# Kernel optimization log

Hardware: AMD Instinct MI355X
Metric: run time of the kernel (lower is better)

Reference implementation:

```python
import jax, jax.numpy as jnp
import numpy as np

B, Z, H, W, C = 8, 16, 32, 32, 512
C8 = C // 8
N = Z * H * W
EPS = 1e-3  # Keras BatchNormalization default epsilon


def setup_inputs() -> dict:
    key = jax.random.key(0)
    ks = jax.random.split(key, 8)
    scale = 0.05
    x = jax.random.normal(ks[0], (B, Z, H, W, C), jnp.float32)
    return {
        "x": x,
        "bn1_gamma": jnp.ones((C,), jnp.float32),
        "bn1_beta": jnp.zeros((C,), jnp.float32),
        "bn1_mean": jax.random.normal(ks[1], (C,), jnp.float32) * 0.1,
        "bn1_var": jnp.abs(jax.random.normal(ks[2], (C,), jnp.float32)) * 0.1 + 1.0,
        "wq": jax.random.normal(ks[3], (C, C8), jnp.float32) * scale,
        "bq": jnp.zeros((C8,), jnp.float32),
        "wk": jax.random.normal(ks[4], (C, C8), jnp.float32) * scale,
        "bk": jnp.zeros((C8,), jnp.float32),
        "wv": jax.random.normal(ks[5], (C, C8), jnp.float32) * scale,
        "bv": jnp.zeros((C8,), jnp.float32),
        "wp": jax.random.normal(ks[6], (C8, C), jnp.float32) * scale,
        "bp": jnp.zeros((C,), jnp.float32),
        "bn2_gamma": jnp.ones((C,), jnp.float32),
        "bn2_beta": jnp.zeros((C,), jnp.float32),
        "bn2_mean": jax.random.normal(ks[7], (C,), jnp.float32) * 0.1,
        "bn2_var": jnp.ones((C,), jnp.float32),
    }


def _bn(t, gamma, beta, mean, var):
    # Keras BatchNormalization (inference), channels-last axis=-1
    return (t - mean) * jax.lax.rsqrt(var + EPS) * gamma + beta


def _conv1x1(t, w, b):
    # 1x1x1 Conv3D == per-voxel channel matmul
    return jnp.einsum('bzhwc,cd->bzhwd', t, w) + b


def reference(x, bn1_gamma, bn1_beta, bn1_mean, bn1_var,
              wq, bq, wk, bk, wv, bv, wp, bp,
              bn2_gamma, bn2_beta, bn2_mean, bn2_var):
    img = _bn(x, bn1_gamma, bn1_beta, bn1_mean, bn1_var)
    q = _conv1x1(img, wq, bq).reshape(B, N, C8)  # (B, N, c)
    k = _conv1x1(img, wk, bk).reshape(B, N, C8)  # (B, N, c)
    v = _conv1x1(img, wv, bv).reshape(B, N, C8)  # (B, N, c)
    # Keras Dot(axes=[1,2])([q, permute(k)]): contracts the N axis of both
    # -> channel Gram matrix s[b,i,j] = sum_n q[b,n,i] * k[b,n,j]
    s = jnp.einsum('bni,bnj->bij', q, k)          # (B, c, c)
    beta = jax.nn.softmax(s, axis=-1)             # (B, c, c)
    # Keras Dot(axes=[1,2])([beta, v]): attn[b,i,j] = sum_m beta[b,m,i] * v[b,j,m]
    attn = jnp.einsum('bmi,bjm->bij', beta, v)    # (B, c, N)
    # Keras Reshape((Z,H,W,c)) on (B, c, N): row-major reinterpretation
    out = attn.reshape(B, Z, H, W, C8)
    out = _conv1x1(out, wp, bp)                   # (B, Z, H, W, C)
    out = _bn(out, bn2_gamma, bn2_beta, bn2_mean, bn2_var)
    return out
```

## Files before the change

kernel.cpp:

```cpp
#include <hip/hip_runtime.h>

#define EPS 1e-3f

typedef _Float16 f16;
typedef _Float16 f16x8 __attribute__((ext_vector_type(8)));
typedef _Float16 f16x4 __attribute__((ext_vector_type(4)));
typedef float f32x4 __attribute__((ext_vector_type(4)));

constexpr int Bn = 8, C = 512, C8 = 64;
constexpr int N = 16384;
constexpr int M = Bn * N;

constexpr size_t OFF_WHI  = 0;
constexpr size_t OFF_WLO  = 196608;
constexpr size_t OFF_BQKV = 327680;
constexpr size_t OFF_WPT  = 328704;
constexpr size_t OFF_BOUT = 394240;
constexpr size_t OFF_V    = 396288;
constexpr size_t OFF_S    = OFF_V + (size_t)M * 64 * 2;
constexpr size_t OFF_BT   = OFF_S + (size_t)8 * 8 * 4096 * 4;

__global__ __launch_bounds__(256) void k0_fold(
    const float* g1, const float* be1, const float* mu1, const float* va1,
    const float* wq, const float* bq, const float* wk, const float* bk,
    const float* wv, const float* bv, const float* wp, const float* bp,
    const float* g2, const float* be2, const float* mu2, const float* va2,
    char* ws)
{
  f16* whi = (f16*)(ws + OFF_WHI);
  f16* wlo = (f16*)(ws + OFF_WLO);
  float* bqkv = (float*)(ws + OFF_BQKV);
  f16* wpt = (f16*)(ws + OFF_WPT);
  float* bout = (float*)(ws + OFF_BOUT);
  float* sbuf = (float*)(ws + OFF_S);
  __shared__ float red[256];
  int blk = blockIdx.x, t = threadIdx.x;
  if (blk < 192) {
    const float* w; const float* bb; int col;
    if (blk < 64)       { w = wq; bb = bq; col = blk; }
    else if (blk < 128) { w = wk; bb = bk; col = blk - 64; }
    else                { w = wv; bb = bv; col = blk - 128; }
    float part = 0.f;
    for (int c = t; c < 512; c += 256) {
      float a1 = g1[c] * rsqrtf(va1[c] + EPS);
      float d1 = be1[c] - mu1[c] * a1;
      float wval = w[c * 64 + col];
      float fw = a1 * wval;
      f16 hi = (f16)fw;
      whi[blk * 512 + c] = hi;
      if (blk < 128) wlo[blk * 512 + c] = (f16)((fw - (float)hi) * 2048.0f);
      part += d1 * wval;
    }
    red[t] = part; __syncthreads();
    for (int s = 128; s > 0; s >>= 1) { if (t < s) red[t] += red[t + s]; __syncthreads(); }
    if (t == 0) bqkv[blk] = red[0] + bb[col];
  } else {
    int co = blk - 192;
    float a2 = g2[co] * rsqrtf(va2[co] + EPS);
    if (t < 64) wpt[co * 64 + t] = (f16)(wp[t * 512 + co] * a2);
    if (t == 0) bout[co] = (bp[co] - mu2[co]) * a2 + be2[co];
    sbuf[co * 512 + t] = 0.0f;
    sbuf[co * 512 + 256 + t] = 0.0f;
  }
}

__global__ __launch_bounds__(256, 2) void k1_qkv(const float* __restrict__ x, char* __restrict__ ws)
{
  const f16* whi = (const f16*)(ws + OFF_WHI);
  const f16* wlo = (const f16*)(ws + OFF_WLO);
  const float* bqkv = (const float*)(ws + OFF_BQKV);
  f16* vbuf  = (f16*)(ws + OFF_V);
  float* spart = (float*)(ws + OFF_S);

  __shared__ f16 xs[2][64 * 72];

  int t = threadIdx.x;
  int wave = t >> 6, lane = t & 63;
  int m0 = blockIdx.x * 64;

  int srow = t >> 2, scol = (t & 3) * 4;
  const float* xg = x + (size_t)(m0 + srow) * 512 + scol;

  int bn0 = wave * 16 + (lane & 15);
  int bn1 = bn0 + 64;
  int bn2 = bn0 + 128;
  int klane = (lane >> 4) * 8;

  f32x4 acc_h[4][2], acc_l[4][2], acc_v[4];
  for (int i = 0; i < 4; i++) {
    for (int j = 0; j < 2; j++) { acc_h[i][j] = (f32x4){0.f,0.f,0.f,0.f}; acc_l[i][j] = (f32x4){0.f,0.f,0.f,0.f}; }
    acc_v[i] = (f32x4){0.f,0.f,0.f,0.f};
  }

  f32x4 a0 = *(const f32x4*)(xg);
  f32x4 a1 = *(const f32x4*)(xg + 16);
  f32x4 a2 = *(const f32x4*)(xg + 32);
  f32x4 a3 = *(const f32x4*)(xg + 48);

  for (int iter = 0; iter < 8; iter++) {
    f16* xb = &xs[iter & 1][0];
    {
      f16x4 h0, h1, h2, h3;
      for (int e = 0; e < 4; e++) { h0[e]=(f16)a0[e]; h1[e]=(f16)a1[e]; h2[e]=(f16)a2[e]; h3[e]=(f16)a3[e]; }
      *(f16x4*)&xb[srow * 72 + scol     ] = h0;
      *(f16x4*)&xb[srow * 72 + scol + 16] = h1;
      *(f16x4*)&xb[srow * 72 + scol + 32] = h2;
      *(f16x4*)&xb[srow * 72 + scol + 48] = h3;
    }
    __syncthreads();
    if (iter < 7) {
      const float* xi = xg + (iter + 1) * 64;
      a0 = *(const f32x4*)(xi);
      a1 = *(const f32x4*)(xi + 16);
      a2 = *(const f32x4*)(xi + 32);
      a3 = *(const f32x4*)(xi + 48);
    }
    for (int ks = 0; ks < 2; ks++) {
      int kg = iter * 64 + ks * 32 + klane;
      f16x8 b0h = *(const f16x8*)(whi + bn0 * 512 + kg);
      f16x8 b1h = *(const f16x8*)(whi + bn1 * 512 + kg);
      f16x8 b2h = *(const f16x8*)(whi + bn2 * 512 + kg);
      f16x8 b0l = *(const f16x8*)(wlo + bn0 * 512 + kg);
      f16x8 b1l = *(const f16x8*)(wlo + bn1 * 512 + kg);
      int aoff = (lane & 15) * 72 + ks * 32 + klane;
      for (int mt = 0; mt < 4; mt++) {
        f16x8 af = *(const f16x8*)&xb[mt * 16 * 72 + aoff];
        acc_h[mt][0] = __builtin_amdgcn_mfma_f32_16x16x32_f16(af, b0h, acc_h[mt][0], 0, 0, 0);
        acc_h[mt][1] = __builtin_amdgcn_mfma_f32_16x16x32_f16(af, b1h, acc_h[mt][1], 0, 0, 0);
        acc_l[mt][0] = __builtin_amdgcn_mfma_f32_16x16x32_f16(af, b0l, acc_l[mt][0], 0, 0, 0);
        acc_l[mt][1] = __builtin_amdgcn_mfma_f32_16x16x32_f16(af, b1l, acc_l[mt][1], 0, 0, 0);
        acc_v[mt]    = __builtin_amdgcn_mfma_f32_16x16x32_f16(af, b2h, acc_v[mt],    0, 0, 0);
      }
    }
  }

  const float inv2048 = 1.0f / 2048.0f;
  float bA = bqkv[bn0], bB = bqkv[bn1], bV = bqkv[bn2];
  f16* qT = &xs[0][0];
  f16* kT = &xs[1][0];
  __syncthreads();
  for (int mt = 0; mt < 4; mt++)
    for (int r = 0; r < 4; r++) {
      int n = (lane >> 4) * 4 + mt * 16 + r;
      size_t row = (size_t)(m0 + n);
      float qv = acc_h[mt][0][r] + acc_l[mt][0][r] * inv2048 + bA;
      float kv = acc_h[mt][1][r] + acc_l[mt][1][r] * inv2048 + bB;
      qT[bn0 * 72 + n] = (f16)qv;
      kT[bn0 * 72 + n] = (f16)kv;
      vbuf[row * 64 + bn0] = (f16)(acc_v[mt][r] + bV);
    }
  __syncthreads();

  f32x4 gacc[4];
  for (int i = 0; i < 4; i++) gacc[i] = (f32x4){0.f,0.f,0.f,0.f};
  for (int ks = 0; ks < 2; ks++) {
    f16x8 bfr = *(const f16x8*)&kT[(wave * 16 + (lane & 15)) * 72 + ks * 32 + klane];
    for (int it = 0; it < 4; it++) {
      f16x8 afr = *(const f16x8*)&qT[(it * 16 + (lane & 15)) * 72 + ks * 32 + klane];
      gacc[it] = __builtin_amdgcn_mfma_f32_16x16x32_f16(afr, bfr, gacc[it], 0, 0, 0);
    }
  }
  int b = blockIdx.x >> 8;
  int g = blockIdx.x & 7;
  float* sdst = spart + ((size_t)(g * 8 + b)) * 4096;
  int j = wave * 16 + (lane & 15);
  for (int it = 0; it < 4; it++)
    for (int r = 0; r < 4; r++) {
      int i = it * 16 + (lane >> 4) * 4 + r;
      atomicAdd(&sdst[i * 64 + j], gacc[it][r]);
    }
}

__global__ __launch_bounds__(256) void k2b_softmax(char* __restrict__ ws)
{
  const float* spart = (const float*)(ws + OFF_S);
  f16* bt = (f16*)(ws + OFF_BT);
  __shared__ float red[64][4];

  int b = blockIdx.x, t = threadIdx.x;
  int m = t & 63, qd = t >> 6;

  float sv[16];
  {
    const float* base = spart + (size_t)b * 4096 + (size_t)m * 64 + qd * 16;
    f32x4 v0 = (f32x4){0.f,0.f,0.f,0.f}, v1 = v0, v2 = v0, v3 = v0;
    for (int g = 0; g < 8; g++) {
      const f32x4* p = (const f32x4*)(base + (size_t)g * 8 * 4096);
      v0 += p[0]; v1 += p[1]; v2 += p[2]; v3 += p[3];
    }
    for (int e = 0; e < 4; e++) { sv[e] = v0[e]; sv[4+e] = v1[e]; sv[8+e] = v2[e]; sv[12+e] = v3[e]; }
  }
  float mx = sv[0];
  for (int jj = 1; jj < 16; jj++) mx = fmaxf(mx, sv[jj]);
  red[m][qd] = mx; __syncthreads();
  float rmx = fmaxf(fmaxf(red[m][0], red[m][1]), fmaxf(red[m][2], red[m][3]));
  __syncthreads();
  float s = 0.f;
  for (int jj = 0; jj < 16; jj++) { float e = __expf(sv[jj] - rmx); sv[jj] = e; s += e; }
  red[m][qd] = s; __syncthreads();
  float inv = 1.0f / (red[m][0] + red[m][1] + red[m][2] + red[m][3]);
  for (int jj = 0; jj < 16; jj++)
    bt[(size_t)b * 4096 + (qd * 16 + jj) * 64 + m] = (f16)(sv[jj] * inv);
}

__device__ __forceinline__ int at_idx(int row, int d) {
  int dd = (d >> 1) ^ (((row >> 3) & 3) << 3);
  return row * 64 + dd * 2 + (d & 1);
}

__global__ __launch_bounds__(256, 2) void k34_attn_proj(char* __restrict__ ws, float* __restrict__ out)
{
  const f16* vbuf = (const f16*)(ws + OFF_V);
  const f16* bt = (const f16*)(ws + OFF_BT);
  const f16* wpt = (const f16*)(ws + OFF_WPT);
  const float* bout = (const float*)(ws + OFF_BOUT);
  __shared__ f16 at[128 * 64];

  int t = threadIdx.x, wave = t >> 6, lane = t & 63;
  int b = blockIdx.x >> 7, jc = blockIdx.x & 127;
  int li = lane & 15;
  int klane = (lane >> 4) * 8;

  f32x4 acc[4][2];
  for (int i = 0; i < 4; i++) for (int j = 0; j < 2; j++) acc[i][j] = (f32x4){0.f,0.f,0.f,0.f};

  for (int km = 0; km < 2; km++) {
    f16x8 af[4], bf[2];
    for (int it = 0; it < 4; it++)
      af[it] = *(const f16x8*)(bt + (size_t)b * 4096 + (it * 16 + li) * 64 + km * 32 + klane);
    for (int jt = 0; jt < 2; jt++) {
      int jrow = jc * 128 + wave * 32 + jt * 16 + li;
      bf[jt] = *(const f16x8*)(vbuf + (size_t)(b * 16384 + jrow) * 64 + km * 32 + klane);
    }
    for (int it = 0; it < 4; it++)
      for (int jt = 0; jt < 2; jt++)
        acc[it][jt] = __builtin_amdgcn_mfma_f32_16x16x32_f16(af[it], bf[jt], acc[it][jt], 0, 0, 0);
  }
  for (int it = 0; it < 4; it++)
    for (int jt = 0; jt < 2; jt++)
      for (int r = 0; r < 4; r++) {
        int i = it * 16 + (lane >> 4) * 4 + r;
        int d = (wave & 1) * 32 + jt * 16 + li;
        at[at_idx(i * 2 + (wave >> 1), d)] = (f16)acc[it][jt][r];
      }
  __syncthreads();

  f16x8 paf[2][2];
  for (int mt = 0; mt < 2; mt++)
    for (int km = 0; km < 2; km++) {
      int row = wave * 32 + mt * 16 + li;
      int d = km * 32 + klane;
      paf[mt][km] = *(const f16x8*)&at[row * 64 + ((((d >> 1) ^ (((row >> 3) & 3) << 3))) << 1)];
    }
  size_t obase = (size_t)b * 16384 * 512;
  for (int strip = 0; strip < 8; strip++) {
    int c0 = strip * 64;
    f16x8 pbf[2][4];
    for (int nt = 0; nt < 4; nt++)
      for (int km = 0; km < 2; km++)
        pbf[km][nt] = *(const f16x8*)(wpt + (size_t)(c0 + nt * 16 + li) * 64 + km * 32 + klane);
    f32x4 pac[2][4];
    for (int mt = 0; mt < 2; mt++) for (int nt = 0; nt < 4; nt++) pac[mt][nt] = (f32x4){0.f,0.f,0.f,0.f};
    for (int km = 0; km < 2; km++)
      for (int mt = 0; mt < 2; mt++)
        for (int nt = 0; nt < 4; nt++)
          pac[mt][nt] = __builtin_amdgcn_mfma_f32_16x16x32_f16(paf[mt][km], pbf[km][nt], pac[mt][nt], 0, 0, 0);
    for (int nt = 0; nt < 4; nt++) {
      int c = c0 + nt * 16 + li;
      float bc = bout[c];
      for (int mt = 0; mt < 2; mt++)
        for (int r = 0; r < 4; r++) {
          int rl = wave * 32 + mt * 16 + (lane >> 4) * 4 + r;
          int pos = (rl >> 1) * 256 + jc * 2 + (rl & 1);
          out[obase + (size_t)pos * 512 + c] = pac[mt][nt][r] + bc;
        }
    }
  }
}

extern "C" void kernel_launch(void* const* d_in, const int* in_sizes, int n_in,
                              void* d_out, int out_size, void* d_ws, size_t ws_size,
                              hipStream_t stream)
{
  const float* x   = (const float*)d_in[0];
  const float* g1  = (const float*)d_in[1];
  const float* be1 = (const float*)d_in[2];
  const float* mu1 = (const float*)d_in[3];
  const float* va1 = (const float*)d_in[4];
  const float* wq  = (const float*)d_in[5];
  const float* bq  = (const float*)d_in[6];
  const float* wk  = (const float*)d_in[7];
  const float* bk  = (const float*)d_in[8];
  const float* wv  = (const float*)d_in[9];
  const float* bv  = (const float*)d_in[10];
  const float* wp  = (const float*)d_in[11];
  const float* bp  = (const float*)d_in[12];
  const float* g2  = (const float*)d_in[13];
  const float* be2 = (const float*)d_in[14];
  const float* mu2 = (const float*)d_in[15];
  const float* va2 = (const float*)d_in[16];
  char* ws = (char*)d_ws;
  float* out = (float*)d_out;

  k0_fold<<<dim3(704), dim3(256), 0, stream>>>(g1, be1, mu1, va1, wq, bq, wk, bk,
                                               wv, bv, wp, bp, g2, be2, mu2, va2, ws);
  k1_qkv<<<dim3(2048), dim3(256), 0, stream>>>(x, ws);
  k2b_softmax<<<dim3(8), dim3(256), 0, stream>>>(ws);
  k34_attn_proj<<<dim3(1024), dim3(256), 0, stream>>>(ws, out);
}
```

Measured before the change: 571.2 us.

## Load x fragments directly into registers in QKV kernel, drop LDS staging

The QKV projection kernel no longer stages x through double-buffered shared memory with barriers. Each lane now loads its MFMA A-fragment straight from global memory and converts it to fp16 in registers, inside a fully unrolled 16-step K loop. Launch bounds are raised to 3 blocks per CU for both the QKV and attention/projection kernels to raise occupancy. The trade-off is less coalesced 32-byte strided global reads with no cross-wave reuse, plus register pressure from the full unroll under a tighter register cap.

```diff
diff --git a/kernel.cpp b/kernel.cpp
--- a/kernel.cpp
+++ b/kernel.cpp
@@ -64,7 +64,7 @@
   }
 }
 
-__global__ __launch_bounds__(256, 2) void k1_qkv(const float* __restrict__ x, char* __restrict__ ws)
+__global__ __launch_bounds__(256, 3) void k1_qkv(const float* __restrict__ x, char* __restrict__ ws)
 {
   const f16* whi = (const f16*)(ws + OFF_WHI);
   const f16* wlo = (const f16*)(ws + OFF_WLO);
@@ -77,14 +77,12 @@
   int t = threadIdx.x;
   int wave = t >> 6, lane = t & 63;
   int m0 = blockIdx.x * 64;
-
-  int srow = t >> 2, scol = (t & 3) * 4;
-  const float* xg = x + (size_t)(m0 + srow) * 512 + scol;
-
-  int bn0 = wave * 16 + (lane & 15);
+  int li = lane & 15;
+  int kl8 = (lane >> 4) * 8;
+
+  int bn0 = wave * 16 + li;
   int bn1 = bn0 + 64;
   int bn2 = bn0 + 128;
-  int klane = (lane >> 4) * 8;
 
   f32x4 acc_h[4][2], acc_l[4][2], acc_v[4];
   for (int i = 0; i < 4; i++) {
@@ -92,45 +90,47 @@
     acc_v[i] = (f32x4){0.f,0.f,0.f,0.f};
   }
 
-  f32x4 a0 = *(const f32x4*)(xg);
-  f32x4 a1 = *(const f32x4*)(xg + 16);
-  f32x4 a2 = *(const f32x4*)(xg + 32);
-  f32x4 a3 = *(const f32x4*)(xg + 48);
-
-  for (int iter = 0; iter < 8; iter++) {
-    f16* xb = &xs[iter & 1][0];
+  const float* xr0 = x + (size_t)(m0 +  0 + li) * 512 + kl8;
+  const float* xr1 = x + (size_t)(m0 + 16 + li) * 512 + kl8;
+  const float* xr2 = x + (size_t)(m0 + 32 + li) * 512 + kl8;
+  const float* xr3 = x + (size_t)(m0 + 48 + li) * 512 + kl8;
+
+  const f16* wb0h = whi + bn0 * 512 + kl8;
+  const f16* wb1h = whi + bn1 * 512 + kl8;
+  const f16* wb2h = whi + bn2 * 512 + kl8;
+  const f16* wb0l = wlo + bn0 * 512 + kl8;
+  const f16* wb1l = wlo + bn1 * 512 + kl8;
+
+#pragma unroll
+  for (int s = 0; s < 16; s++) {
+    const int kg = s * 32;
+    f16x8 b0h = *(const f16x8*)(wb0h + kg);
+    f16x8 b1h = *(const f16x8*)(wb1h + kg);
+    f16x8 b2h = *(const f16x8*)(wb2h + kg);
+    f16x8 b0l = *(const f16x8*)(wb0l + kg);
+    f16x8 b1l = *(const f16x8*)(wb1l + kg);
+
+    f16x8 af[4];
     {
-      f16x4 h0, h1, h2, h3;
-      for (int e = 0; e < 4; e++) { h0[e]=(f16)a0[e]; h1[e]=(f16)a1[e]; h2[e]=(f16)a2[e]; h3[e]=(f16)a3[e]; }
-      *(f16x4*)&xb[srow * 72 + scol     ] = h0;
-      *(f16x4*)&xb[srow * 72 + scol + 16] = h1;
-      *(f16x4*)&xb[srow * 72 + scol + 32] = h2;
-      *(f16x4*)&xb[srow * 72 + scol + 48] = h3;
-    }
-    __syncthreads();
-    if (iter < 7) {
-      const float* xi = xg + (iter + 1) * 64;
-      a0 = *(const f32x4*)(xi);
-      a1 = *(const f32x4*)(xi + 16);
-      a2 = *(const f32x4*)(xi + 32);
-      a3 = *(const f32x4*)(xi + 48);
-    }
-    for (int ks = 0; ks < 2; ks++) {
-      int kg = iter * 64 + ks * 32 + klane;
-      f16x8 b0h = *(const f16x8*)(whi + bn0 * 512 + kg);
-      f16x8 b1h = *(const f16x8*)(whi + bn1 * 512 + kg);
-      f16x8 b2h = *(const f16x8*)(whi + bn2 * 512 + kg);
-      f16x8 b0l = *(const f16x8*)(wlo + bn0 * 512 + kg);
-      f16x8 b1l = *(const f16x8*)(wlo + bn1 * 512 + kg);
-      int aoff = (lane & 15) * 72 + ks * 32 + klane;
-      for (int mt = 0; mt < 4; mt++) {
-        f16x8 af = *(const f16x8*)&xb[mt * 16 * 72 + aoff];
-        acc_h[mt][0] = __builtin_amdgcn_mfma_f32_16x16x32_f16(af, b0h, acc_h[mt][0], 0, 0, 0);
-        acc_h[mt][1] = __builtin_amdgcn_mfma_f32_16x16x32_f16(af, b1h, acc_h[mt][1], 0, 0, 0);
-        acc_l[mt][0] = __builtin_amdgcn_mfma_f32_16x16x32_f16(af, b0l, acc_l[mt][0], 0, 0, 0);
-        acc_l[mt][1] = __builtin_amdgcn_mfma_f32_16x16x32_f16(af, b1l, acc_l[mt][1], 0, 0, 0);
-        acc_v[mt]    = __builtin_amdgcn_mfma_f32_16x16x32_f16(af, b2h, acc_v[mt],    0, 0, 0);
+      f32x4 r00 = *(const f32x4*)(xr0 + kg), r01 = *(const f32x4*)(xr0 + kg + 4);
+      f32x4 r10 = *(const f32x4*)(xr1 + kg), r11 = *(const f32x4*)(xr1 + kg + 4);
+      f32x4 r20 = *(const f32x4*)(xr2 + kg), r21 = *(const f32x4*)(xr2 + kg + 4);
+      f32x4 r30 = *(const f32x4*)(xr3 + kg), r31 = *(const f32x4*)(xr3 + kg + 4);
+#pragma unroll
+      for (int e = 0; e < 4; e++) {
+        af[0][e] = (f16)r00[e]; af[0][e + 4] = (f16)r01[e];
+        af[1][e] = (f16)r10[e]; af[1][e + 4] = (f16)r11[e];
+        af[2][e] = (f16)r20[e]; af[2][e + 4] = (f16)r21[e];
+        af[3][e] = (f16)r30[e]; af[3][e + 4] = (f16)r31[e];
       }
+    }
+#pragma unroll
+    for (int mt = 0; mt < 4; mt++) {
+      acc_h[mt][0] = __builtin_amdgcn_mfma_f32_16x16x32_f16(af[mt], b0h, acc_h[mt][0], 0, 0, 0);
+      acc_h[mt][1] = __builtin_amdgcn_mfma_f32_16x16x32_f16(af[mt], b1h, acc_h[mt][1], 0, 0, 0);
+      acc_l[mt][0] = __builtin_amdgcn_mfma_f32_16x16x32_f16(af[mt], b0l, acc_l[mt][0], 0, 0, 0);
+      acc_l[mt][1] = __builtin_amdgcn_mfma_f32_16x16x32_f16(af[mt], b1l, acc_l[mt][1], 0, 0, 0);
+      acc_v[mt]    = __builtin_amdgcn_mfma_f32_16x16x32_f16(af[mt], b2h, acc_v[mt],    0, 0, 0);
     }
   }
 
@@ -138,7 +138,6 @@
   float bA = bqkv[bn0], bB = bqkv[bn1], bV = bqkv[bn2];
   f16* qT = &xs[0][0];
   f16* kT = &xs[1][0];
-  __syncthreads();
   for (int mt = 0; mt < 4; mt++)
     for (int r = 0; r < 4; r++) {
       int n = (lane >> 4) * 4 + mt * 16 + r;
@@ -154,16 +153,16 @@
   f32x4 gacc[4];
   for (int i = 0; i < 4; i++) gacc[i] = (f32x4){0.f,0.f,0.f,0.f};
   for (int ks = 0; ks < 2; ks++) {
-    f16x8 bfr = *(const f16x8*)&kT[(wave * 16 + (lane & 15)) * 72 + ks * 32 + klane];
+    f16x8 bfr = *(const f16x8*)&kT[(wave * 16 + li) * 72 + ks * 32 + kl8];
     for (int it = 0; it < 4; it++) {
-      f16x8 afr = *(const f16x8*)&qT[(it * 16 + (lane & 15)) * 72 + ks * 32 + klane];
+      f16x8 afr = *(const f16x8*)&qT[(it * 16 + li) * 72 + ks * 32 + kl8];
       gacc[it] = __builtin_amdgcn_mfma_f32_16x16x32_f16(afr, bfr, gacc[it], 0, 0, 0);
     }
   }
   int b = blockIdx.x >> 8;
   int g = blockIdx.x & 7;
   float* sdst = spart + ((size_t)(g * 8 + b)) * 4096;
-  int j = wave * 16 + (lane & 15);
+  int j = wave * 16 + li;
   for (int it = 0; it < 4; it++)
     for (int r = 0; r < 4; r++) {
       int i = it * 16 + (lane >> 4) * 4 + r;
@@ -208,7 +207,7 @@
   return row * 64 + dd * 2 + (d & 1);
 }
 
-__global__ __launch_bounds__(256, 2) void k34_attn_proj(char* __restrict__ ws, float* __restrict__ out)
+__global__ __launch_bounds__(256, 3) void k34_attn_proj(char* __restrict__ ws, float* __restrict__ out)
 {
   const f16* vbuf = (const f16*)(ws + OFF_V);
   const f16* bt = (const f16*)(ws + OFF_BT);
```

New measurement: 670.0 us. +17.3%, slower.
